# Optimization experiments

Measured on AMD Instinct MI355X. Metric: run time of the kernel, lower is better.

## Reference

```python
import jax, jax.numpy as jnp
import numpy as np

N_NODES = 50000
IN_CH, HID, OUT_CH = 512, 128, 64
N_EDGES = 800000


def gcn_conv(x, edge_index, W, b, num_nodes):
    # PyG GCNConv: add self-loops, symmetric deg^{-1/2} normalization,
    # linear transform then scatter-add aggregation at target nodes.
    row, col = edge_index[0], edge_index[1]
    loop = jnp.arange(num_nodes, dtype=row.dtype)
    rows = jnp.concatenate([row, loop])  # sources
    cols = jnp.concatenate([col, loop])  # targets
    deg = jax.ops.segment_sum(jnp.ones_like(cols, dtype=x.dtype), cols, num_segments=num_nodes)
    dinv = jnp.where(deg > 0, jax.lax.rsqrt(deg), 0.0)
    norm = dinv[rows] * dinv[cols]  # [E+N]
    h = x @ W  # [N, out]
    msg = norm[:, None] * h[rows]  # gather + scale
    out = jax.ops.segment_sum(msg, cols, num_segments=num_nodes)
    return out + b


def setup_inputs() -> dict:
    key = jax.random.key(0)
    k = jax.random.split(key, 8)
    x = jax.random.normal(k[0], (N_NODES, IN_CH), dtype=jnp.float32)
    pos_edge_index = jax.random.randint(k[1], (2, N_EDGES), 0, N_NODES, dtype=jnp.int64 if jax.config.jax_enable_x64 else jnp.int32)
    neg_edge_index = jax.random.randint(k[2], (2, N_EDGES), 0, N_NODES, dtype=pos_edge_index.dtype)
    # Glorot-ish init for weights, zeros for bias (PyG default)
    W1 = jax.random.normal(k[3], (IN_CH, HID), dtype=jnp.float32) * (1.0 / np.sqrt(IN_CH))
    b1 = jnp.zeros((HID,), dtype=jnp.float32)
    W2 = jax.random.normal(k[4], (HID, OUT_CH), dtype=jnp.float32) * (1.0 / np.sqrt(HID))
    b2 = jnp.zeros((OUT_CH,), dtype=jnp.float32)
    return {"x": x, "pos_edge_index": pos_edge_index, "neg_edge_index": neg_edge_index,
            "W1": W1, "b1": b1, "W2": W2, "b2": b2}


def reference(x, pos_edge_index, neg_edge_index, W1, b1, W2, b2):
    n = x.shape[0]
    h = gcn_conv(x, pos_edge_index, W1, b1, n)
    h = jax.nn.relu(h)
    z = gcn_conv(h, pos_edge_index, W2, b2, n)  # encode
    edge_index = jnp.concatenate([pos_edge_index, neg_edge_index], axis=-1)
    # decode: per-edge dot product of endpoint embeddings
    logits = jnp.sum(z[edge_index[0]] * z[edge_index[1]], axis=-1)
    return logits
```

## Files before the change

### kernel.cpp

```cpp
#include <hip/hip_runtime.h>

#define WAVE 64
#define CAP 64

typedef __bf16 v8bf __attribute__((ext_vector_type(8)));
typedef __bf16 v4bf __attribute__((ext_vector_type(4)));
typedef __bf16 v2bf __attribute__((ext_vector_type(2)));
typedef float f32x4 __attribute__((ext_vector_type(4)));

__device__ __forceinline__ void cvt8(const f32x4& u, const f32x4& v, v8bf& h, v8bf& l) {
    float f[8] = {u.x, u.y, u.z, u.w, v.x, v.y, v.z, v.w};
#pragma unroll
    for (int j = 0; j < 8; ++j) {
        __bf16 hh = (__bf16)f[j];
        h[j] = hh;
        l[j] = (__bf16)(f[j] - (float)hh);
    }
}

__global__ __launch_bounds__(256) void prep_kernel(const float* __restrict__ W1,
                                                   const float* __restrict__ W2,
                                                   __bf16* __restrict__ Wt1hi,
                                                   __bf16* __restrict__ Wt1lo,
                                                   __bf16* __restrict__ Wt2hi,
                                                   __bf16* __restrict__ Wt2lo) {
    int b = blockIdx.x;
    int tid = threadIdx.x;
    if (b < 256) {
        int idx = b * 256 + tid;
        int k = idx >> 7, n = idx & 127;
        float v = W1[idx];
        __bf16 h = (__bf16)v;
        Wt1hi[n * 512 + k] = h;
        Wt1lo[n * 512 + k] = (__bf16)(v - (float)h);
    } else {
        int idx = (b - 256) * 256 + tid;
        int k = idx >> 6, n = idx & 63;
        float v = W2[idx];
        __bf16 h = (__bf16)v;
        int o = (k >> 5) * (64 * 32) + n * 32 + (k & 31);
        Wt2hi[o] = h;
        Wt2lo[o] = (__bf16)(v - (float)h);
    }
}

template <int NC, int KK, bool OBF16, bool FILL>
__global__ __launch_bounds__(256, 3) void gemm_fill_kernel(
    const float* __restrict__ A, const __bf16* __restrict__ Bhi,
    const __bf16* __restrict__ Blo, void* __restrict__ Cout, int M, int NG,
    const int* __restrict__ ei, int E, int* __restrict__ cursor,
    int* __restrict__ srcs) {
    constexpr int BK = 32;
    constexpr int LD = 40;
    constexpr int NT = NC / 16;
    constexpr int CPT = (NC * 4) / 256;

    __shared__ __bf16 sAhi[128][LD];
    __shared__ __bf16 sAlo[128][LD];
    __shared__ __bf16 sBhi[NC][LD];
    __shared__ __bf16 sBlo[NC][LD];

    const int tid = threadIdx.x;

    if (FILL && blockIdx.x >= NG) {
        int bb = (blockIdx.x - NG) * 512;
#pragma unroll
        for (int j = 0; j < 2; ++j) {
            int e = bb + tid + j * 256;
            if (e < E) {
                int dst = ei[E + e];
                int p = atomicAdd(&cursor[dst], 1);
                if (p < CAP) srcs[(size_t)dst * CAP + p] = ei[e];
            }
        }
        return;
    }

    const int lane = tid & 63;
    const int wv = tid >> 6;
    const int ln15 = lane & 15;
    const int quad = lane >> 4;
    const int rowBase = blockIdx.x * 128;

    const int sr = tid >> 1;
    const int kh = (tid & 1) * 16;
    const int gr = rowBase + sr;
    const bool aval = gr < M;
    const float* aBase = A + (size_t)gr * KK + kh;

    int bcol[CPT], bg[CPT];
#pragma unroll
    for (int c = 0; c < CPT; ++c) {
        int chunk = tid * CPT + c;
        bcol[c] = chunk >> 2;
        bg[c] = chunk & 3;
    }

    f32x4 acc[2][NT];
#pragma unroll
    for (int rt = 0; rt < 2; ++rt)
#pragma unroll
        for (int t = 0; t < NT; ++t) acc[rt][t] = (f32x4){0.f, 0.f, 0.f, 0.f};

    float4 aR[4];
    v8bf bhR[CPT], blR[CPT];

    auto loadTiles = [&](int k0) {
        if (aval) {
#pragma unroll
            for (int q = 0; q < 4; ++q) aR[q] = *(const float4*)(aBase + k0 + q * 4);
        } else {
#pragma unroll
            for (int q = 0; q < 4; ++q) aR[q] = make_float4(0.f, 0.f, 0.f, 0.f);
        }
#pragma unroll
        for (int c = 0; c < CPT; ++c) {
            bhR[c] = *(const v8bf*)(Bhi + (size_t)bcol[c] * KK + k0 + bg[c] * 8);
            blR[c] = *(const v8bf*)(Blo + (size_t)bcol[c] * KK + k0 + bg[c] * 8);
        }
    };

    loadTiles(0);

    for (int k0 = 0; k0 < KK; k0 += BK) {
        float fv[16];
#pragma unroll
        for (int q = 0; q < 4; ++q) {
            fv[q * 4 + 0] = aR[q].x; fv[q * 4 + 1] = aR[q].y;
            fv[q * 4 + 2] = aR[q].z; fv[q * 4 + 3] = aR[q].w;
        }
#pragma unroll
        for (int g = 0; g < 2; ++g) {
            v8bf hv, lv;
#pragma unroll
            for (int j = 0; j < 8; ++j) {
                float v = fv[g * 8 + j];
                __bf16 h = (__bf16)v;
                hv[j] = h;
                lv[j] = (__bf16)(v - (float)h);
            }
            *(v8bf*)&sAhi[sr][kh + g * 8] = hv;
            *(v8bf*)&sAlo[sr][kh + g * 8] = lv;
        }
#pragma unroll
        for (int c = 0; c < CPT; ++c) {
            *(v8bf*)&sBhi[bcol[c]][bg[c] * 8] = bhR[c];
            *(v8bf*)&sBlo[bcol[c]][bg[c] * 8] = blR[c];
        }
        __syncthreads();

        if (k0 + BK < KK) loadTiles(k0 + BK);

        v8bf ah[2], al[2];
#pragma unroll
        for (int rt = 0; rt < 2; ++rt) {
            int r = wv * 32 + rt * 16 + ln15;
            ah[rt] = *(const v8bf*)&sAhi[r][quad * 8];
            al[rt] = *(const v8bf*)&sAlo[r][quad * 8];
        }
#pragma unroll
        for (int t = 0; t < NT; ++t) {
            v8bf bh = *(const v8bf*)&sBhi[t * 16 + ln15][quad * 8];
            v8bf bl = *(const v8bf*)&sBlo[t * 16 + ln15][quad * 8];
#pragma unroll
            for (int rt = 0; rt < 2; ++rt) {
                acc[rt][t] = __builtin_amdgcn_mfma_f32_16x16x32_bf16(ah[rt], bh, acc[rt][t], 0, 0, 0);
                acc[rt][t] = __builtin_amdgcn_mfma_f32_16x16x32_bf16(al[rt], bh, acc[rt][t], 0, 0, 0);
                acc[rt][t] = __builtin_amdgcn_mfma_f32_16x16x32_bf16(ah[rt], bl, acc[rt][t], 0, 0, 0);
            }
        }
        __syncthreads();
    }

#pragma unroll
    for (int rt = 0; rt < 2; ++rt) {
#pragma unroll
        for (int r = 0; r < 4; ++r) {
            int grow = rowBase + wv * 32 + rt * 16 + quad * 4 + r;
            if (grow < M) {
#pragma unroll
                for (int t = 0; t < NT; ++t) {
                    float v = acc[rt][t][r];
                    if (OBF16)
                        ((__bf16*)Cout)[(size_t)grow * NC + t * 16 + ln15] = (__bf16)v;
                    else
                        ((float*)Cout)[(size_t)grow * NC + t * 16 + ln15] = v;
                }
            }
        }
    }
}

__global__ __launch_bounds__(256) void gather1_gemm2_kernel(
    const __bf16* __restrict__ hs, const int* __restrict__ counts,
    const int* __restrict__ srcs, const float* __restrict__ bias,
    const __bf16* __restrict__ W2hi, const __bf16* __restrict__ W2lo,
    __bf16* __restrict__ hs2, int N) {
    constexpr int LDO = 132;
    __shared__ float out1[16 * LDO];

    const int tid = threadIdx.x;
    const int lane = tid & 63;
    const int wv = tid >> 6;
    const int base = blockIdx.x * 16;

    for (int i = 0; i < 4; ++i) {
        int slot = wv * 4 + i;
        int node = base + slot;
        float v0 = 0.f, v1 = 0.f;
        int col = 2 * lane;
        if (node < N) {
            int cnt = counts[node];
            if (cnt > CAP) cnt = CAP;
            int beg = node * CAP;
            int end = beg + cnt;
            float dn = rsqrtf((float)cnt + 1.0f);
            float a0, a1;
            {
                v2bf s = *(const v2bf*)&hs[(size_t)node * 128 + col];
                a0 = dn * (float)s[0];
                a1 = dn * (float)s[1];
            }
            int e = beg;
            for (; e + 4 <= end; e += 4) {
                int s0 = srcs[e], s1 = srcs[e + 1], s2 = srcs[e + 2], s3 = srcs[e + 3];
                float d0 = rsqrtf((float)counts[s0] + 1.0f);
                float d1 = rsqrtf((float)counts[s1] + 1.0f);
                float d2 = rsqrtf((float)counts[s2] + 1.0f);
                float d3 = rsqrtf((float)counts[s3] + 1.0f);
                v2bf r0 = *(const v2bf*)&hs[(size_t)s0 * 128 + col];
                v2bf r1 = *(const v2bf*)&hs[(size_t)s1 * 128 + col];
                v2bf r2 = *(const v2bf*)&hs[(size_t)s2 * 128 + col];
                v2bf r3 = *(const v2bf*)&hs[(size_t)s3 * 128 + col];
                a0 += d0 * (float)r0[0] + d1 * (float)r1[0] + d2 * (float)r2[0] + d3 * (float)r3[0];
                a1 += d0 * (float)r0[1] + d1 * (float)r1[1] + d2 * (float)r2[1] + d3 * (float)r3[1];
            }
            for (; e < end; ++e) {
                int s0 = srcs[e];
                float d0 = rsqrtf((float)counts[s0] + 1.0f);
                v2bf r0 = *(const v2bf*)&hs[(size_t)s0 * 128 + col];
                a0 += d0 * (float)r0[0];
                a1 += d0 * (float)r0[1];
            }
            float2 bv = *(const float2*)&bias[col];
            v0 = fmaxf(dn * a0 + bv.x, 0.f);
            v1 = fmaxf(dn * a1 + bv.y, 0.f);
        }
        *(float2*)&out1[slot * LDO + col] = make_float2(v0, v1);
    }
    __syncthreads();

    const int ln15 = lane & 15;
    const int quad = lane >> 4;
    f32x4 acc = (f32x4){0.f, 0.f, 0.f, 0.f};
#pragma unroll
    for (int kc = 0; kc < 4; ++kc) {
        const float* ap = &out1[ln15 * LDO + kc * 32 + quad * 8];
        f32x4 u = *(const f32x4*)(ap);
        f32x4 v = *(const f32x4*)(ap + 4);
        v8bf ah, al;
        cvt8(u, v, ah, al);
        size_t bo = (size_t)kc * (64 * 32) + (wv * 16 + ln15) * 32 + quad * 8;
        v8bf bh = *(const v8bf*)(W2hi + bo);
        v8bf bl = *(const v8bf*)(W2lo + bo);
        acc = __builtin_amdgcn_mfma_f32_16x16x32_bf16(ah, bh, acc, 0, 0, 0);
        acc = __builtin_amdgcn_mfma_f32_16x16x32_bf16(al, bh, acc, 0, 0, 0);
        acc = __builtin_amdgcn_mfma_f32_16x16x32_bf16(ah, bl, acc, 0, 0, 0);
    }
#pragma unroll
    for (int r = 0; r < 4; ++r) {
        int node = base + quad * 4 + r;
        if (node < N) hs2[(size_t)node * 64 + wv * 16 + ln15] = (__bf16)acc[r];
    }
}

template <int F, bool RELU, bool BF16OUT>
__global__ __launch_bounds__(256) void gather_agg_bf16(const __bf16* __restrict__ hs,
                                                       const int* __restrict__ counts,
                                                       const int* __restrict__ srcs,
                                                       const float* __restrict__ bias,
                                                       void* __restrict__ outp, int N) {
    int node = blockIdx.x * 4 + (int)(threadIdx.x >> 6);
    if (node >= N) return;
    int lane = threadIdx.x & 63;
    int cnt = counts[node];
    if (cnt > CAP) cnt = CAP;
    int beg = node * CAP;
    int end = beg + cnt;
    float dn = rsqrtf((float)cnt + 1.0f);

    int q = lane >> 4;
    int sl = lane & 15;
    int col = sl * 4;
    float a0 = 0.f, a1 = 0.f, a2 = 0.f, a3 = 0.f;
    if (q == 0) {
        v4bf s = *(const v4bf*)&hs[(size_t)node * F + col];
        a0 = dn * (float)s[0]; a1 = dn * (float)s[1];
        a2 = dn * (float)s[2]; a3 = dn * (float)s[3];
    }
    int e = beg + q;
    for (; e + 4 < end; e += 8) {
        int s0 = srcs[e], s1 = srcs[e + 4];
        float d0 = rsqrtf((float)counts[s0] + 1.0f);
        float d1 = rsqrtf((float)counts[s1] + 1.0f);
        v4bf r0 = *(const v4bf*)&hs[(size_t)s0 * F + col];
        v4bf r1 = *(const v4bf*)&hs[(size_t)s1 * F + col];
        a0 += d0 * (float)r0[0] + d1 * (float)r1[0];
        a1 += d0 * (float)r0[1] + d1 * (float)r1[1];
        a2 += d0 * (float)r0[2] + d1 * (float)r1[2];
        a3 += d0 * (float)r0[3] + d1 * (float)r1[3];
    }
    if (e < end) {
        int s0 = srcs[e];
        float d0 = rsqrtf((float)counts[s0] + 1.0f);
        v4bf r0 = *(const v4bf*)&hs[(size_t)s0 * F + col];
        a0 += d0 * (float)r0[0]; a1 += d0 * (float)r0[1];
        a2 += d0 * (float)r0[2]; a3 += d0 * (float)r0[3];
    }
    a0 += __shfl_xor(a0, 16); a0 += __shfl_xor(a0, 32);
    a1 += __shfl_xor(a1, 16); a1 += __shfl_xor(a1, 32);
    a2 += __shfl_xor(a2, 16); a2 += __shfl_xor(a2, 32);
    a3 += __shfl_xor(a3, 16); a3 += __shfl_xor(a3, 32);
    if (q == 0) {
        float4 bv = *(const float4*)&bias[col];
        float v0 = dn * a0 + bv.x;
        float v1 = dn * a1 + bv.y;
        float v2 = dn * a2 + bv.z;
        float v3 = dn * a3 + bv.w;
        if (RELU) {
            v0 = fmaxf(v0, 0.f); v1 = fmaxf(v1, 0.f);
            v2 = fmaxf(v2, 0.f); v3 = fmaxf(v3, 0.f);
        }
        if (BF16OUT) {
            v4bf o;
            o[0] = (__bf16)v0; o[1] = (__bf16)v1;
            o[2] = (__bf16)v2; o[3] = (__bf16)v3;
            *(v4bf*)&((__bf16*)outp)[(size_t)node * F + col] = o;
        } else {
            *(float4*)&((float*)outp)[(size_t)node * F + col] =
                make_float4(v0, v1, v2, v3);
        }
    }
}

__global__ __launch_bounds__(256) void decode_bf16_kernel(const __bf16* __restrict__ z,
                                                          const int* __restrict__ pos,
                                                          const int* __restrict__ neg, int E,
                                                          float* __restrict__ out) {
    int tid = blockIdx.x * blockDim.x + threadIdx.x;
    int g = tid >> 2;
    int l = tid & 3;
    int total = 2 * E;
    if (g >= total) return;
    int src, dst;
    if (g < E) {
        src = pos[g];
        dst = pos[E + g];
    } else {
        int e = g - E;
        src = neg[e];
        dst = neg[E + e];
    }
    const __bf16* zs = z + (size_t)src * 64 + l * 16;
    const __bf16* zd = z + (size_t)dst * 64 + l * 16;
    v8bf a0 = *(const v8bf*)zs;
    v8bf a1 = *(const v8bf*)(zs + 8);
    v8bf b0 = *(const v8bf*)zd;
    v8bf b1 = *(const v8bf*)(zd + 8);
    float p = 0.f;
#pragma unroll
    for (int j = 0; j < 8; ++j) p += (float)a0[j] * (float)b0[j] + (float)a1[j] * (float)b1[j];
    p += __shfl_xor(p, 1);
    p += __shfl_xor(p, 2);
    if (l == 0) out[g] = p;
}

extern "C" void kernel_launch(void* const* d_in, const int* in_sizes, int n_in, void* d_out,
                              int out_size, void* d_ws, size_t ws_size, hipStream_t stream) {
    const float* x = (const float*)d_in[0];
    const int* pos_ei = (const int*)d_in[1];
    const int* neg_ei = (const int*)d_in[2];
    const float* W1 = (const float*)d_in[3];
    const float* b1 = (const float*)d_in[4];
    const float* W2 = (const float*)d_in[5];
    const float* b2 = (const float*)d_in[6];
    float* out = (float*)d_out;

    const int IN = 512, HID = 128, OUT = 64;
    const int N = in_sizes[0] / IN;
    const int E = in_sizes[1] / 2;

    size_t nAlign = ((size_t)N + 255) & ~(size_t)255;
    float* p = (float*)d_ws;
    __bf16* hs1 = (__bf16*)p; p += (size_t)N * HID / 2;
    __bf16* hs2 = (__bf16*)p; p += (size_t)N * OUT / 2;
    __bf16* zbf = (__bf16*)p; p += (size_t)N * OUT / 2;
    int* cursor = (int*)p; p += nAlign;
    int* srcs = (int*)p; p += (size_t)N * CAP;
    __bf16* Wt1hi = (__bf16*)p; p += (size_t)IN * HID / 2;
    __bf16* Wt1lo = (__bf16*)p; p += (size_t)IN * HID / 2;
    __bf16* Wt2hi = (__bf16*)p; p += (size_t)HID * OUT / 2;
    __bf16* Wt2lo = (__bf16*)p; p += (size_t)HID * OUT / 2;

    const int NG = (N + 127) / 128;
    const int NF = (E + 511) / 512;

    hipMemsetAsync(cursor, 0, (size_t)N * sizeof(int), stream);
    prep_kernel<<<288, 256, 0, stream>>>(W1, W2, Wt1hi, Wt1lo, Wt2hi, Wt2lo);

    gemm_fill_kernel<128, 512, true, true><<<NG + NF, 256, 0, stream>>>(
        x, Wt1hi, Wt1lo, hs1, N, NG, pos_ei, E, cursor, srcs);

    gather1_gemm2_kernel<<<(N + 15) / 16, 256, 0, stream>>>(
        hs1, cursor, srcs, b1, Wt2hi, Wt2lo, hs2, N);

    gather_agg_bf16<64, false, true>
        <<<(N + 3) / 4, 256, 0, stream>>>(hs2, cursor, srcs, b2, zbf, N);

    decode_bf16_kernel<<<((size_t)2 * E * 4 + 255) / 256, 256, 0, stream>>>(
        zbf, pos_ei, neg_ei, E, out);
}
```

Baseline: 315.6 us.

## Load A fragments directly to registers and double-buffer B via async LDS loads

```diff
diff --git a/kernel.cpp b/kernel.cpp
--- a/kernel.cpp
+++ b/kernel.cpp
@@ -8,7 +8,22 @@
 typedef __bf16 v2bf __attribute__((ext_vector_type(2)));
 typedef float f32x4 __attribute__((ext_vector_type(4)));
 
+__device__ __forceinline__ void async16(void* lds, const void* g) {
+    __builtin_amdgcn_global_load_lds((const __attribute__((address_space(1))) void*)g,
+                                     (__attribute__((address_space(3))) void*)lds, 16, 0, 0);
+}
+
 __device__ __forceinline__ void cvt8(const f32x4& u, const f32x4& v, v8bf& h, v8bf& l) {
+    float f[8] = {u.x, u.y, u.z, u.w, v.x, v.y, v.z, v.w};
+#pragma unroll
+    for (int j = 0; j < 8; ++j) {
+        __bf16 hh = (__bf16)f[j];
+        h[j] = hh;
+        l[j] = (__bf16)(f[j] - (float)hh);
+    }
+}
+
+__device__ __forceinline__ void cvt8f(const float4& u, const float4& v, v8bf& h, v8bf& l) {
     float f[8] = {u.x, u.y, u.z, u.w, v.x, v.y, v.z, v.w};
 #pragma unroll
     for (int j = 0; j < 8; ++j) {
@@ -51,14 +66,11 @@
     const int* __restrict__ ei, int E, int* __restrict__ cursor,
     int* __restrict__ srcs) {
     constexpr int BK = 32;
-    constexpr int LD = 40;
     constexpr int NT = NC / 16;
-    constexpr int CPT = (NC * 4) / 256;
-
-    __shared__ __bf16 sAhi[128][LD];
-    __shared__ __bf16 sAlo[128][LD];
-    __shared__ __bf16 sBhi[NC][LD];
-    __shared__ __bf16 sBlo[NC][LD];
+    constexpr int NIT = KK / BK;
+    constexpr int NCH = NC / 16;
+
+    __shared__ __bf16 sB[2][2][NC * BK];
 
     const int tid = threadIdx.x;
 
@@ -82,19 +94,25 @@
     const int quad = lane >> 4;
     const int rowBase = blockIdx.x * 128;
 
-    const int sr = tid >> 1;
-    const int kh = (tid & 1) * 16;
-    const int gr = rowBase + sr;
-    const bool aval = gr < M;
-    const float* aBase = A + (size_t)gr * KK + kh;
-
-    int bcol[CPT], bg[CPT];
-#pragma unroll
-    for (int c = 0; c < CPT; ++c) {
-        int chunk = tid * CPT + c;
-        bcol[c] = chunk >> 2;
-        bg[c] = chunk & 3;
-    }
+    const int brow = lane >> 2;
+    const int bslot = lane & 3;
+    auto stageB = [&](int buf, int k0) {
+#pragma unroll
+        for (int i = 0; i < NCH / 4; ++i) {
+            int c = wv * (NCH / 4) + i;
+            int row = c * 16 + brow;
+            int gk = k0 + ((bslot ^ (row & 3)) << 3);
+            async16(&sB[buf][0][c * 512], Bhi + (size_t)row * KK + gk);
+            async16(&sB[buf][1][c * 512], Blo + (size_t)row * KK + gk);
+        }
+    };
+
+    int r0 = rowBase + wv * 32 + ln15;
+    int r1 = r0 + 16;
+    if (r0 > M - 1) r0 = M - 1;
+    if (r1 > M - 1) r1 = M - 1;
+    const float* aP0 = A + (size_t)r0 * KK + quad * 8;
+    const float* aP1 = A + (size_t)r1 * KK + quad * 8;
 
     f32x4 acc[2][NT];
 #pragma unroll
@@ -103,73 +121,46 @@
         for (int t = 0; t < NT; ++t) acc[rt][t] = (f32x4){0.f, 0.f, 0.f, 0.f};
 
     float4 aR[4];
-    v8bf bhR[CPT], blR[CPT];
-
-    auto loadTiles = [&](int k0) {
-        if (aval) {
-#pragma unroll
-            for (int q = 0; q < 4; ++q) aR[q] = *(const float4*)(aBase + k0 + q * 4);
-        } else {
-#pragma unroll
-            for (int q = 0; q < 4; ++q) aR[q] = make_float4(0.f, 0.f, 0.f, 0.f);
-        }
-#pragma unroll
-        for (int c = 0; c < CPT; ++c) {
-            bhR[c] = *(const v8bf*)(Bhi + (size_t)bcol[c] * KK + k0 + bg[c] * 8);
-            blR[c] = *(const v8bf*)(Blo + (size_t)bcol[c] * KK + k0 + bg[c] * 8);
-        }
-    };
-
-    loadTiles(0);
-
-    for (int k0 = 0; k0 < KK; k0 += BK) {
-        float fv[16];
-#pragma unroll
-        for (int q = 0; q < 4; ++q) {
-            fv[q * 4 + 0] = aR[q].x; fv[q * 4 + 1] = aR[q].y;
-            fv[q * 4 + 2] = aR[q].z; fv[q * 4 + 3] = aR[q].w;
-        }
-#pragma unroll
-        for (int g = 0; g < 2; ++g) {
-            v8bf hv, lv;
-#pragma unroll
-            for (int j = 0; j < 8; ++j) {
-                float v = fv[g * 8 + j];
-                __bf16 h = (__bf16)v;
-                hv[j] = h;
-                lv[j] = (__bf16)(v - (float)h);
-            }
-            *(v8bf*)&sAhi[sr][kh + g * 8] = hv;
-            *(v8bf*)&sAlo[sr][kh + g * 8] = lv;
-        }
-#pragma unroll
-        for (int c = 0; c < CPT; ++c) {
-            *(v8bf*)&sBhi[bcol[c]][bg[c] * 8] = bhR[c];
-            *(v8bf*)&sBlo[bcol[c]][bg[c] * 8] = blR[c];
-        }
+    aR[0] = *(const float4*)(aP0);
+    aR[1] = *(const float4*)(aP0 + 4);
+    aR[2] = *(const float4*)(aP1);
+    aR[3] = *(const float4*)(aP1 + 4);
+
+    stageB(0, 0);
+    __syncthreads();
+
+    int cur = 0;
+    for (int ks = 0; ks < NIT; ++ks) {
+        if (ks + 1 < NIT) stageB(cur ^ 1, (ks + 1) * BK);
+
+        v8bf ah[2], al[2];
+        cvt8f(aR[0], aR[1], ah[0], al[0]);
+        cvt8f(aR[2], aR[3], ah[1], al[1]);
+        if (ks + 1 < NIT) {
+            aP0 += BK;
+            aP1 += BK;
+            aR[0] = *(const float4*)(aP0);
+            aR[1] = *(const float4*)(aP0 + 4);
+            aR[2] = *(const float4*)(aP1);
+            aR[3] = *(const float4*)(aP1 + 4);
+        }
+
+#pragma unroll
+        for (int t = 0; t < NT; ++t) {
+            int row = t * 16 + ln15;
+            int off = row * BK + ((quad ^ (row & 3)) << 3);
+            v8bf bh = *(const v8bf*)&sB[cur][0][off];
+            v8bf bl = *(const v8bf*)&sB[cur][1][off];
+            acc[0][t] = __builtin_amdgcn_mfma_f32_16x16x32_bf16(ah[0], bh, acc[0][t], 0, 0, 0);
+            acc[0][t] = __builtin_amdgcn_mfma_f32_16x16x32_bf16(al[0], bh, acc[0][t], 0, 0, 0);
+            acc[0][t] = __builtin_amdgcn_mfma_f32_16x16x32_bf16(ah[0], bl, acc[0][t], 0, 0, 0);
+            acc[1][t] = __builtin_amdgcn_mfma_f32_16x16x32_bf16(ah[1], bh, acc[1][t], 0, 0, 0);
+            acc[1][t] = __builtin_amdgcn_mfma_f32_16x16x32_bf16(al[1], bh, acc[1][t], 0, 0, 0);
+            acc[1][t] = __builtin_amdgcn_mfma_f32_16x16x32_bf16(ah[1], bl, acc[1][t], 0, 0, 0);
+        }
+
         __syncthreads();
-
-        if (k0 + BK < KK) loadTiles(k0 + BK);
-
-        v8bf ah[2], al[2];
-#pragma unroll
-        for (int rt = 0; rt < 2; ++rt) {
-            int r = wv * 32 + rt * 16 + ln15;
-            ah[rt] = *(const v8bf*)&sAhi[r][quad * 8];
-            al[rt] = *(const v8bf*)&sAlo[r][quad * 8];
-        }
-#pragma unroll
-        for (int t = 0; t < NT; ++t) {
-            v8bf bh = *(const v8bf*)&sBhi[t * 16 + ln15][quad * 8];
-            v8bf bl = *(const v8bf*)&sBlo[t * 16 + ln15][quad * 8];
-#pragma unroll
-            for (int rt = 0; rt < 2; ++rt) {
-                acc[rt][t] = __builtin_amdgcn_mfma_f32_16x16x32_bf16(ah[rt], bh, acc[rt][t], 0, 0, 0);
-                acc[rt][t] = __builtin_amdgcn_mfma_f32_16x16x32_bf16(al[rt], bh, acc[rt][t], 0, 0, 0);
-                acc[rt][t] = __builtin_amdgcn_mfma_f32_16x16x32_bf16(ah[rt], bl, acc[rt][t], 0, 0, 0);
-            }
-        }
-        __syncthreads();
+        cur ^= 1;
     }
 
 #pragma unroll
```

Measured after the change: 315.8 us. No clear change (+0.1%).
